# Performance work log

Measured on AMD Instinct MI355X. Metric: run time of the kernel, lower is better.

The kernel has to match this reference:

```python
import jax, jax.numpy as jnp
import numpy as np

# EISANI constants (inference path, dense non-EI weights, static connections)
NUM_BITS = 16        # EISANITABcontinuousVarEncodingNumBits
K_SYN = 32           # numberOfSynapsesPerSegment
SEGMENTS = 2         # numberOfSegmentsPerNeuron
THETA = 8            # segment activation threshold (synapse-count based)
H = 4096             # hiddenLayerSize
F = 128              # numberOfFeatures
C = 10               # numberOfClasses
B = 64               # batch


def _make_weight(key, h, s, p):
    """Dense weight [h, s, p] with exactly K_SYN nonzero +/-1 synapses per segment
    (mirrors _initialise_layer_weights dense non-EI branch)."""
    k1, k2 = jax.random.split(key)
    cols = jax.random.randint(k1, (h, s, K_SYN), 0, p)
    signs = jnp.where(jax.random.bernoulli(k2, 0.5, (h, s, K_SYN)), 1.0, -1.0).astype(jnp.float32)
    hh = jnp.arange(h)[:, None, None]
    ss = jnp.arange(s)[None, :, None]
    return jnp.zeros((h, s, p), jnp.float32).at[hh, ss, cols].set(signs)


def setup_inputs() -> dict:
    key = jax.random.key(0)
    kx, k0, k1, k2, ko = jax.random.split(key, 5)
    x = jax.random.uniform(kx, (B, F), dtype=jnp.float32)
    W0 = _make_weight(k0, H, SEGMENTS, F * NUM_BITS)
    W1 = _make_weight(k1, H, SEGMENTS, H)
    W2 = _make_weight(k2, H, SEGMENTS, H)
    outW = jax.random.normal(ko, (3, H, C), dtype=jnp.float32) * 0.02
    return {"x": x, "W0": W0, "W1": W1, "W2": W2, "outW": outW}


def _encode(x):
    # thermometer (graded) encoding of continuous vars into NUM_BITS binary bits
    thresholds = (jnp.arange(NUM_BITS, dtype=jnp.float32) + 1.0) / (NUM_BITS + 1.0)
    bits = (x[:, :, None] >= thresholds).astype(jnp.float32)  # [B, F, NUM_BITS]
    return bits.reshape(x.shape[0], -1)  # [B, F*NUM_BITS]


def reference(x, W0, W1, W2, outW):
    acts = _encode(x)  # [B, P0]
    layer_acts = []
    for W in (W0, W1, W2):
        # segment membrane sums over binary presynaptic activations
        z = jnp.einsum('bp,hsp->bhs', acts, W)  # [B, H, S]
        # neuron fires if ANY segment reaches threshold
        fired = jnp.any(z >= THETA, axis=-1)
        acts = fired.astype(jnp.float32)  # binary activation [B, H]
        layer_acts.append(acts)
    stacked = jnp.stack(layer_acts)  # [L, B, H]
    out = jnp.einsum('lbh,lhc->bc', stacked, outW)  # class scores [B, C]
    return out
```

## Files before the change

kernel.cpp:

```cpp
#include <hip/hip_runtime.h>
#include <hip/hip_bf16.h>

typedef unsigned long long u64;

#define H_SZ 4096
#define NBITS 16
#define NFEAT 128
#define NCLS 10
#define THETA 8


__global__ void encode_kernel(const float* __restrict__ x, u64* __restrict__ actp0) {
    int idx = blockIdx.x * blockDim.x + threadIdx.x;
    if (idx >= 32 * 64) return;
    int wword = idx >> 6;
    int b = idx & 63;
    int c = wword >> 2, j = wword & 3;
    u64 word = 0;
    for (int i = 0; i < 64; i++) {
        int p = c * 256 + 4 * i + j;
        int f = p >> 4, t = p & 15;
        float thr = (t + 1.0f) / (NBITS + 1.0f);
        if (x[b * NFEAT + f] >= thr) word |= (1ULL << i);
    }
    actp0[wword * 64 + b] = word;
}

template <int P>
__global__ __launch_bounds__(256) void layer_kernel(const float* __restrict__ W,
                                                    const u64* __restrict__ actp,
                                                    u64* __restrict__ ballots) {
    constexpr int NW = P / 64;
    __shared__ u64 lds[NW * 64];
    int tid = threadIdx.x;
    for (int i = tid; i < NW * 64; i += 256) lds[i] = actp[i];
    __syncthreads();

    int lane = tid & 63;
    int warp = tid >> 6;
    #pragma unroll
    for (int r = 0; r < 2; r++) {
        int wid = (blockIdx.x * 4 + warp) * 2 + r;
        const float4* wrow = (const float4*)(W + (size_t)wid * P) + lane;
        unsigned int zp = 0, zn = 0;
        #pragma unroll
        for (int c = 0; c < P / 256; c++) {
            float4 w = wrow[c * 64];
            u64 p0 = __ballot(w.x > 0.0f);
            u64 n0 = __ballot(w.x < 0.0f);
            u64 p1 = __ballot(w.y > 0.0f);
            u64 n1 = __ballot(w.y < 0.0f);
            u64 p2 = __ballot(w.z > 0.0f);
            u64 n2 = __ballot(w.z < 0.0f);
            u64 p3 = __ballot(w.w > 0.0f);
            u64 n3 = __ballot(w.w < 0.0f);
            u64 a0 = lds[(c * 4 + 0) * 64 + lane];
            u64 a1 = lds[(c * 4 + 1) * 64 + lane];
            u64 a2 = lds[(c * 4 + 2) * 64 + lane];
            u64 a3 = lds[(c * 4 + 3) * 64 + lane];
            zp += __builtin_popcountll(a0 & p0) + __builtin_popcountll(a1 & p1)
                + __builtin_popcountll(a2 & p2) + __builtin_popcountll(a3 & p3);
            zn += __builtin_popcountll(a0 & n0) + __builtin_popcountll(a1 & n1)
                + __builtin_popcountll(a2 & n2) + __builtin_popcountll(a3 & n3);
        }
        int z = (int)zp - (int)zn;
        u64 fz = __ballot(z >= THETA);
        if (lane == 0) ballots[wid] = fz;
    }
}

__global__ void transpose_kernel(const u64* __restrict__ ballots,
                                 u64* __restrict__ f,
                                 u64* __restrict__ actp) {
    __shared__ u64 lds[256];
    int c = blockIdx.x;
    int tid = threadIdx.x;
    int h = c * 256 + tid;
    u64 fh = ballots[2 * h] | ballots[2 * h + 1];
    f[h] = fh;
    lds[tid] = fh;
    __syncthreads();
    int j = tid >> 6, b = tid & 63;
    u64 word = 0;
    #pragma unroll 8
    for (int i = 0; i < 64; i++)
        word |= ((lds[4 * i + j] >> b) & 1ULL) << i;
    actp[(c * 4 + j) * 64 + b] = word;
}

__global__ void output_kernel(const float* __restrict__ outW,
                              const u64* __restrict__ f,
                              float* __restrict__ out) {
    int tid = threadIdx.x;
    int lane = tid & 63;
    int wid = blockIdx.x * 4 + (tid >> 6);
    int l = wid / (NCLS * 64);
    int rem = wid % (NCLS * 64);
    int c = rem / 64;
    int chunk = rem % 64;
    const u64* fl = f + l * H_SZ;
    int h0 = chunk * 64;
    float acc = 0.0f;
    #pragma unroll 8
    for (int h = h0; h < h0 + 64; h++) {
        float wv = outW[((size_t)(l * H_SZ + h)) * NCLS + c];
        u64 ball = fl[h];
        if ((ball >> lane) & 1ULL) acc += wv;
    }
    atomicAdd(&out[lane * NCLS + c], acc);
}

extern "C" void kernel_launch(void* const* d_in, const int* in_sizes, int n_in,
                              void* d_out, int out_size, void* d_ws, size_t ws_size,
                              hipStream_t stream) {
    const float* x    = (const float*)d_in[0];
    const float* W0   = (const float*)d_in[1];
    const float* W1   = (const float*)d_in[2];
    const float* W2   = (const float*)d_in[3];
    const float* outW = (const float*)d_in[4];
    float* out = (float*)d_out;

    char* ws = (char*)d_ws;
    u64* actp0   = (u64*)(ws);
    u64* actp1   = (u64*)(ws + 16384);
    u64* actp2   = (u64*)(ws + 49152);
    u64* ballots = (u64*)(ws + 81920);
    u64* f       = (u64*)(ws + 147456);
    u64* scratch = (u64*)(ws + 245760);

    hipMemsetAsync(d_out, 0, (size_t)out_size * sizeof(float), stream);

    encode_kernel<<<8, 256, 0, stream>>>(x, actp0);

    layer_kernel<2048><<<1024, 256, 0, stream>>>(W0, actp0, ballots);
    transpose_kernel<<<16, 256, 0, stream>>>(ballots, f + 0 * H_SZ, actp1);

    layer_kernel<4096><<<1024, 256, 0, stream>>>(W1, actp1, ballots);
    transpose_kernel<<<16, 256, 0, stream>>>(ballots, f + 1 * H_SZ, actp2);

    layer_kernel<4096><<<1024, 256, 0, stream>>>(W2, actp2, ballots);
    transpose_kernel<<<16, 256, 0, stream>>>(ballots, f + 2 * H_SZ, scratch);

    output_kernel<<<480, 256, 0, stream>>>(outW, f, out);
}
```

Baseline: 394.4 us.

## Split weight sign extraction into separate bitmask conversion kernels before layer evaluation

Adds a convert kernel that ballots each dense float weight row into positive and negative 64-bit sign masks stored in workspace. Layer kernels then read only the compact masks and popcount them against the packed activations, with one segment per wave instead of two. This spreads the ballot-heavy conversion across many more waves and leaves the layer pass latency-light. In exchange it adds extra launches and mask write/read traffic.

```diff
diff --git a/kernel.cpp b/kernel.cpp
--- a/kernel.cpp
+++ b/kernel.cpp
@@ -26,47 +26,59 @@
     actp0[wword * 64 + b] = word;
 }
 
-template <int P>
-__global__ __launch_bounds__(256) void layer_kernel(const float* __restrict__ W,
-                                                    const u64* __restrict__ actp,
-                                                    u64* __restrict__ ballots) {
-    constexpr int NW = P / 64;
-    __shared__ u64 lds[NW * 64];
+__global__ __launch_bounds__(256) void convert_kernel(const float* __restrict__ W,
+                                                      u64* __restrict__ masks) {
+    int lane = threadIdx.x & 63;
+    int wave = blockIdx.x * 4 + (threadIdx.x >> 6);
+    #pragma unroll
+    for (int k = 0; k < 4; k++) {
+        int c = wave * 4 + k;
+        float4 v = ((const float4*)W)[(size_t)c * 64 + lane];
+        u64 m0 = __ballot(v.x > 0.0f);
+        u64 m1 = __ballot(v.x < 0.0f);
+        u64 m2 = __ballot(v.y > 0.0f);
+        u64 m3 = __ballot(v.y < 0.0f);
+        u64 m4 = __ballot(v.z > 0.0f);
+        u64 m5 = __ballot(v.z < 0.0f);
+        u64 m6 = __ballot(v.w > 0.0f);
+        u64 m7 = __ballot(v.w < 0.0f);
+        u64 w = m0;
+        w = (lane == 1) ? m1 : w;
+        w = (lane == 2) ? m2 : w;
+        w = (lane == 3) ? m3 : w;
+        w = (lane == 4) ? m4 : w;
+        w = (lane == 5) ? m5 : w;
+        w = (lane == 6) ? m6 : w;
+        w = (lane == 7) ? m7 : w;
+        if (lane < 8) masks[(size_t)c * 8 + lane] = w;
+    }
+}
+
+template <int NC>
+__global__ __launch_bounds__(256) void layer_mask_kernel(const u64* __restrict__ masks,
+                                                         const u64* __restrict__ actp,
+                                                         u64* __restrict__ ballots) {
+    __shared__ u64 lds[NC * 4 * 64];
     int tid = threadIdx.x;
-    for (int i = tid; i < NW * 64; i += 256) lds[i] = actp[i];
+    for (int i = tid; i < NC * 4 * 64; i += 256) lds[i] = actp[i];
     __syncthreads();
 
     int lane = tid & 63;
-    int warp = tid >> 6;
+    int wid = blockIdx.x * 4 + (tid >> 6);
+    const u64* mrow = masks + (size_t)wid * (NC * 8);
+    int z = 0;
     #pragma unroll
-    for (int r = 0; r < 2; r++) {
-        int wid = (blockIdx.x * 4 + warp) * 2 + r;
-        const float4* wrow = (const float4*)(W + (size_t)wid * P) + lane;
-        unsigned int zp = 0, zn = 0;
+    for (int c = 0; c < NC; c++) {
         #pragma unroll
-        for (int c = 0; c < P / 256; c++) {
-            float4 w = wrow[c * 64];
-            u64 p0 = __ballot(w.x > 0.0f);
-            u64 n0 = __ballot(w.x < 0.0f);
-            u64 p1 = __ballot(w.y > 0.0f);
-            u64 n1 = __ballot(w.y < 0.0f);
-            u64 p2 = __ballot(w.z > 0.0f);
-            u64 n2 = __ballot(w.z < 0.0f);
-            u64 p3 = __ballot(w.w > 0.0f);
-            u64 n3 = __ballot(w.w < 0.0f);
-            u64 a0 = lds[(c * 4 + 0) * 64 + lane];
-            u64 a1 = lds[(c * 4 + 1) * 64 + lane];
-            u64 a2 = lds[(c * 4 + 2) * 64 + lane];
-            u64 a3 = lds[(c * 4 + 3) * 64 + lane];
-            zp += __builtin_popcountll(a0 & p0) + __builtin_popcountll(a1 & p1)
-                + __builtin_popcountll(a2 & p2) + __builtin_popcountll(a3 & p3);
-            zn += __builtin_popcountll(a0 & n0) + __builtin_popcountll(a1 & n1)
-                + __builtin_popcountll(a2 & n2) + __builtin_popcountll(a3 & n3);
+        for (int j = 0; j < 4; j++) {
+            u64 p = mrow[c * 8 + j * 2];
+            u64 n = mrow[c * 8 + j * 2 + 1];
+            u64 a = lds[(c * 4 + j) * 64 + lane];
+            z += __builtin_popcountll(a & p) - __builtin_popcountll(a & n);
         }
-        int z = (int)zp - (int)zn;
-        u64 fz = __ballot(z >= THETA);
-        if (lane == 0) ballots[wid] = fz;
     }
+    u64 fz = __ballot(z >= THETA);
+    if (lane == 0) ballots[wid] = fz;
 }
 
 __global__ void transpose_kernel(const u64* __restrict__ ballots,
@@ -127,18 +139,25 @@
     u64* ballots = (u64*)(ws + 81920);
     u64* f       = (u64*)(ws + 147456);
     u64* scratch = (u64*)(ws + 245760);
+    u64* mask0   = (u64*)(ws + (1u << 20));
+    u64* mask1   = (u64*)(ws + (6u << 20));
+    u64* mask2   = (u64*)(ws + (15u << 20));
 
     hipMemsetAsync(d_out, 0, (size_t)out_size * sizeof(float), stream);
 
     encode_kernel<<<8, 256, 0, stream>>>(x, actp0);
 
-    layer_kernel<2048><<<1024, 256, 0, stream>>>(W0, actp0, ballots);
+    convert_kernel<<<4096, 256, 0, stream>>>(W0, mask0);
+    convert_kernel<<<8192, 256, 0, stream>>>(W1, mask1);
+    convert_kernel<<<8192, 256, 0, stream>>>(W2, mask2);
+
+    layer_mask_kernel<8><<<2048, 256, 0, stream>>>(mask0, actp0, ballots);
     transpose_kernel<<<16, 256, 0, stream>>>(ballots, f + 0 * H_SZ, actp1);
 
-    layer_kernel<4096><<<1024, 256, 0, stream>>>(W1, actp1, ballots);
+    layer_mask_kernel<16><<<2048, 256, 0, stream>>>(mask1, actp1, ballots);
     transpose_kernel<<<16, 256, 0, stream>>>(ballots, f + 1 * H_SZ, actp2);
 
-    layer_kernel<4096><<<1024, 256, 0, stream>>>(W2, actp2, ballots);
+    layer_mask_kernel<16><<<2048, 256, 0, stream>>>(mask2, actp2, ballots);
     transpose_kernel<<<16, 256, 0, stream>>>(ballots, f + 2 * H_SZ, scratch);
 
     output_kernel<<<480, 256, 0, stream>>>(outW, f, out);
```

Measured after the change: 454.5 us. 15.2% more time.
